# Performance work log

Hardware: AMD Instinct MI355X
Metric: run time of the kernel (lower is better)

Reference implementation:

```python
import jax, jax.numpy as jnp
import numpy as np

N = 100000      # nodes
E = 800000      # directed edges (avg in-degree 8)
FIN = 2         # node features: [type, requests]
C = 32          # embedding_size (per-head out channels)
H = 4           # heads
HC = H * C      # 128
L = 3           # extra conv layers after conv1
D1, D2 = 128, 64
NL = 15         # num_locations
BN_EPS = 1e-5


def _tconv(x, src, dst, ea, qw, qb, kw, kb, vw, vb, ew, skw, skb, bw):
    """PyG TransformerConv with heads=H, concat=True, beta=True, edge_dim."""
    n = x.shape[0]
    q = (x @ qw.T + qb).reshape(n, H, C)
    k = (x @ kw.T + kb).reshape(n, H, C)
    v = (x @ vw.T + vb).reshape(n, H, C)
    e = (ea @ ew.T).reshape(-1, H, C)                     # [E,H,C], lin_edge has no bias
    ke = k[src] + e
    alpha = (q[dst] * ke).sum(-1) / jnp.sqrt(jnp.float32(C))   # [E,H]
    # scatter-softmax over incoming edges of each destination node
    amax = jax.ops.segment_max(alpha, dst, num_segments=n)     # [N,H]
    ex = jnp.exp(alpha - amax[dst])
    denom = jax.ops.segment_sum(ex, dst, num_segments=n)
    attn = ex / jnp.where(denom > 0, denom, 1.0)[dst]
    msg = (v[src] + e) * attn[..., None]                       # [E,H,C]
    out = jax.ops.segment_sum(msg, dst, num_segments=n).reshape(n, HC)
    skip = x @ skw.T + skb                                     # root transform
    beta = jax.nn.sigmoid(jnp.concatenate([out, skip, out - skip], -1) @ bw.T)  # [N,1]
    return beta * skip + (1.0 - beta) * out


def _bn(x, g, b):
    # BatchNorm1d with batch statistics (biased variance), as in torch training math
    mu = x.mean(0)
    var = ((x - mu) ** 2).mean(0)
    return (x - mu) / jnp.sqrt(var + BN_EPS) * g + b


def _forward(node_type, requests, latency, active_mask, edge_index, P):
    (q1_w, q1_b, k1_w, k1_b, v1_w, v1_b, e1_w, skip1_w, skip1_b, beta1_w,
     transf1_w, transf1_b, bn1_g, bn1_b,
     qL_w, qL_b, kL_w, kL_b, vL_w, vL_b, eL_w, skipL_w, skipL_b, betaL_w,
     transfL_w, transfL_b, bnL_g, bnL_b,
     lin1_w, lin1_b, lin2_w, lin2_b, rem_w, rem_b, addp_w, addp_b) = P
    src, dst = edge_index[0], edge_index[1]
    ea = latency[:, None]                                  # [E,1]
    x = jnp.stack([node_type, requests], 1)                # [N,2]
    x = _tconv(x, src, dst, ea, q1_w, q1_b, k1_w, k1_b, v1_w, v1_b,
               e1_w, skip1_w, skip1_b, beta1_w)
    x = _bn(jax.nn.relu(x @ transf1_w.T + transf1_b), bn1_g, bn1_b)
    for i in range(L):
        x = _tconv(x, src, dst, ea, qL_w[i], qL_b[i], kL_w[i], kL_b[i], vL_w[i], vL_b[i],
                   eL_w[i], skipL_w[i], skipL_b[i], betaL_w[i])
        x = _bn(jax.nn.relu(x @ transfL_w[i].T + transfL_b[i]), bnL_g[i], bnL_b[i])
    x = jax.nn.relu(x @ lin1_w.T + lin1_b)                 # dropout(p=0.8) is eval no-op
    x = jax.nn.relu(x @ lin2_w.T + lin2_b)                 # [N,D2]
    mask = active_mask
    head = mask[:NL]
    rm_head = jnp.where(head == 0.0, -jnp.inf, jnp.where(jnp.isneginf(head), 0.0, head))
    remove_mask = mask.at[:NL].set(rm_head)
    removed_logits = (x @ rem_w.T + rem_b)[:, 0] + remove_mask   # [N]
    k1, k2 = jax.random.split(jax.random.key(42))
    action1 = jax.random.categorical(k1, removed_logits)
    mask2 = mask.at[action1].set(0.0)
    proj = jnp.tanh(x[action1] @ addp_w.T + addp_b)              # [D2]
    new_logits = x @ proj + mask2                                # [N]
    action2 = jax.random.categorical(k2, new_logits)
    return removed_logits, new_logits, action1, action2


def setup_inputs() -> dict:
    key = jax.random.key(0)
    ks = iter(jax.random.split(key, 80))
    def nrm(shape, s=0.1):
        return jax.random.normal(next(ks), shape, jnp.float32) * s
    inp = {
        "node_type": jax.random.uniform(next(ks), (N,), jnp.float32),
        "requests": jax.random.uniform(next(ks), (N,), jnp.float32),
        "latency": jax.random.uniform(next(ks), (E,), jnp.float32),
        "active_mask": jnp.zeros((N,), jnp.float32),
        "edge_index": jax.random.randint(next(ks), (2, E), 0, N, dtype=jnp.int32),
        "q1_w": nrm((HC, FIN)), "q1_b": jnp.zeros((HC,)),
        "k1_w": nrm((HC, FIN)), "k1_b": jnp.zeros((HC,)),
        "v1_w": nrm((HC, FIN)), "v1_b": jnp.zeros((HC,)),
        "e1_w": nrm((HC, 1)),
        "skip1_w": nrm((HC, FIN)), "skip1_b": jnp.zeros((HC,)),
        "beta1_w": nrm((1, 3 * HC)),
        "transf1_w": nrm((C, HC)), "transf1_b": jnp.zeros((C,)),
        "bn1_g": jnp.ones((C,)), "bn1_b": jnp.zeros((C,)),
        "qL_w": nrm((L, HC, C)), "qL_b": jnp.zeros((L, HC)),
        "kL_w": nrm((L, HC, C)), "kL_b": jnp.zeros((L, HC)),
        "vL_w": nrm((L, HC, C)), "vL_b": jnp.zeros((L, HC)),
        "eL_w": nrm((L, HC, 1)),
        "skipL_w": nrm((L, HC, C)), "skipL_b": jnp.zeros((L, HC)),
        "betaL_w": nrm((L, 1, 3 * HC)),
        "transfL_w": nrm((L, C, HC)), "transfL_b": jnp.zeros((L, C)),
        "bnL_g": jnp.ones((L, C)), "bnL_b": jnp.zeros((L, C)),
        "lin1_w": nrm((D1, C)), "lin1_b": jnp.zeros((D1,)),
        "lin2_w": nrm((D2, D1)), "lin2_b": jnp.zeros((D2,)),
        "rem_w": nrm((1, D2)), "rem_b": jnp.zeros((1,)),
        "addp_w": nrm((D2, D2)), "addp_b": jnp.zeros((D2,)),
    }
    return inp


def reference(node_type, requests, latency, active_mask, edge_index,
              q1_w, q1_b, k1_w, k1_b, v1_w, v1_b, e1_w, skip1_w, skip1_b, beta1_w,
              transf1_w, transf1_b, bn1_g, bn1_b,
              qL_w, qL_b, kL_w, kL_b, vL_w, vL_b, eL_w, skipL_w, skipL_b, betaL_w,
              transfL_w, transfL_b, bnL_g, bnL_b,
              lin1_w, lin1_b, lin2_w, lin2_b, rem_w, rem_b, addp_w, addp_b):
    P = (q1_w, q1_b, k1_w, k1_b, v1_w, v1_b, e1_w, skip1_w, skip1_b, beta1_w,
         transf1_w, transf1_b, bn1_g, bn1_b,
         qL_w, qL_b, kL_w, kL_b, vL_w, vL_b, eL_w, skipL_w, skipL_b, betaL_w,
         transfL_w, transfL_b, bnL_g, bnL_b,
         lin1_w, lin1_b, lin2_w, lin2_b, rem_w, rem_b, addp_w, addp_b)
    rl, nl, a1, a2 = _forward(node_type, requests, latency, active_mask, edge_index, P)
    log_probs = jnp.stack([jax.nn.log_softmax(rl)[a1], jax.nn.log_softmax(nl)[a2]])
    logits = jnp.stack([rl, nl])      # [2,N]
    actions = jnp.stack([a1, a2])     # [2]
    return logits, actions, log_probs
```

## Files before the change

### kernel.cpp

```cpp
#include <hip/hip_runtime.h>
#include <hip/hip_bf16.h>
#include <math.h>
#include <stdint.h>
#include <limits.h>

#define NN 100000
#define NE 800000
#define PB 512
#define NDB 512
#define NEGBIG (-1e30f)

typedef __hip_bfloat16 bf16;

__device__ __forceinline__ float bf2f(unsigned short u)
{
  union { unsigned v; float f; } x; x.v = ((unsigned)u) << 16; return x.f;
}
__device__ __forceinline__ unsigned short f2bf(float f)
{
  bf16 h = __float2bfloat16(f);
  return *reinterpret_cast<unsigned short*>(&h);
}

__device__ __forceinline__ uint2 tf_dev(unsigned k0, unsigned k1, unsigned x0, unsigned x1)
{
  const unsigned ks2 = k0 ^ k1 ^ 0x1BD11BDAu;
#define TFR(r) { x0 += x1; x1 = (x1 << r) | (x1 >> (32 - r)); x1 ^= x0; }
  x0 += k0; x1 += k1;
  TFR(13) TFR(15) TFR(26) TFR(6)
  x0 += k1; x1 += ks2 + 1u;
  TFR(17) TFR(29) TFR(16) TFR(24)
  x0 += ks2; x1 += k0 + 2u;
  TFR(13) TFR(15) TFR(26) TFR(6)
  x0 += k0; x1 += k1 + 3u;
  TFR(17) TFR(29) TFR(16) TFR(24)
  x0 += k1; x1 += ks2 + 4u;
  TFR(13) TFR(15) TFR(26) TFR(6)
  x0 += ks2; x1 += k0 + 5u;
#undef TFR
  return make_uint2(x0, x1);
}

static void tf_host(unsigned k0, unsigned k1, unsigned x0, unsigned x1,
                    unsigned* o0, unsigned* o1)
{
  const unsigned ks2 = k0 ^ k1 ^ 0x1BD11BDAu;
#define TFR(r) { x0 += x1; x1 = (x1 << r) | (x1 >> (32 - r)); x1 ^= x0; }
  x0 += k0; x1 += k1;
  TFR(13) TFR(15) TFR(26) TFR(6)
  x0 += k1; x1 += ks2 + 1u;
  TFR(17) TFR(29) TFR(16) TFR(24)
  x0 += ks2; x1 += k0 + 2u;
  TFR(13) TFR(15) TFR(26) TFR(6)
  x0 += k0; x1 += k1 + 3u;
  TFR(17) TFR(29) TFR(16) TFR(24)
  x0 += k1; x1 += ks2 + 4u;
  TFR(13) TFR(15) TFR(26) TFR(6)
  x0 += ks2; x1 += k0 + 5u;
#undef TFR
  *o0 = x0; *o1 = x1;
}

__device__ __forceinline__ float gumbel_of(unsigned ka, unsigned kb, int i)
{
  uint2 c = tf_dev(ka, kb, 0u, (unsigned)i);
  unsigned bits = c.x ^ c.y;
  float f = __uint_as_float((bits >> 9) | 0x3f800000u) - 1.0f;
  const float TINYF = 1.17549435e-38f;
  float u = fmaxf(TINYF, f + TINYF);
  return -logf(-logf(u));
}

__global__ __launch_bounds__(256) void k_zero2(int* __restrict__ a, int* __restrict__ b)
{
  int i = blockIdx.x * 256 + threadIdx.x;
  if (i < NN) { a[i] = 0; b[i] = 0; }
}

__global__ __launch_bounds__(256) void k_hist(const int* __restrict__ edst, int* __restrict__ deg)
{
  int e = blockIdx.x * 256 + threadIdx.x;
  if (e < NE) atomicAdd(&deg[edst[e]], 1);
}

__global__ __launch_bounds__(1024) void k_scan(const int* __restrict__ deg, int* __restrict__ rowptr)
{
  __shared__ int wsum[16];
  __shared__ int chtot;
  const int t = threadIdx.x;
  const int lane = t & 63;
  const int wv = t >> 6;
  int carry = 0;
  for (int base = 0; base < NN; base += 4096) {
    int i0 = base + t * 4;
    int d0 = 0, d1 = 0, d2 = 0, d3 = 0;
    if (i0 + 3 < NN) { int4 dd = *(const int4*)(deg + i0); d0 = dd.x; d1 = dd.y; d2 = dd.z; d3 = dd.w; }
    else {
      if (i0     < NN) d0 = deg[i0];
      if (i0 + 1 < NN) d1 = deg[i0 + 1];
      if (i0 + 2 < NN) d2 = deg[i0 + 2];
      if (i0 + 3 < NN) d3 = deg[i0 + 3];
    }
    int tsum = d0 + d1 + d2 + d3;
    int sc = tsum;
    #pragma unroll
    for (int off = 1; off < 64; off <<= 1) { int o = __shfl_up(sc, off); if (lane >= off) sc += o; }
    if (lane == 63) wsum[wv] = sc;
    __syncthreads();
    if (wv == 0 && lane < 16) {
      int wval = wsum[lane];
      int wsc = wval;
      #pragma unroll
      for (int off = 1; off < 16; off <<= 1) { int o = __shfl_up(wsc, off); if (lane >= off) wsc += o; }
      if (lane == 15) chtot = wsc;
      wsum[lane] = wsc - wval;
    }
    __syncthreads();
    int excl = carry + wsum[wv] + (sc - tsum);
    if (i0     < NN) rowptr[i0]     = excl;
    if (i0 + 1 < NN) rowptr[i0 + 1] = excl + d0;
    if (i0 + 2 < NN) rowptr[i0 + 2] = excl + d0 + d1;
    if (i0 + 3 < NN) rowptr[i0 + 3] = excl + d0 + d1 + d2;
    carry += chtot;
    __syncthreads();
  }
  if (t == 0) rowptr[NN] = carry;
}

__global__ __launch_bounds__(256) void k_scatter(
    const int* __restrict__ esrc, const int* __restrict__ edst,
    const float* __restrict__ lat, const int* __restrict__ rowptr,
    int* __restrict__ fill, int2* __restrict__ csr)
{
  int e = blockIdx.x * 256 + threadIdx.x;
  if (e >= NE) return;
  int d = edst[e];
  int pos = rowptr[d] + atomicAdd(&fill[d], 1);
  csr[pos] = make_int2(esrc[e], __float_as_int(lat[e]));
}

__global__ __launch_bounds__(256) void k_qkvs_first(
    const float* __restrict__ nt, const float* __restrict__ rq,
    const float* __restrict__ qw, const float* __restrict__ qbv,
    const float* __restrict__ kw, const float* __restrict__ kbv,
    const float* __restrict__ vw, const float* __restrict__ vbv,
    const float* __restrict__ sw, const float* __restrict__ sbv,
    float* __restrict__ q, unsigned short* __restrict__ kv, float* __restrict__ sk)
{
  int idx = blockIdx.x * 256 + threadIdx.x;
  if (idx >= NN * 64) return;
  int n = idx >> 6, l = idx & 63;
  int j0 = 2 * l, j1 = 2 * l + 1;
  float a = nt[n], b = rq[n];
  float2 qo;
  qo.x = (a * qw[2 * j0] + b * qw[2 * j0 + 1]) + qbv[j0];
  qo.y = (a * qw[2 * j1] + b * qw[2 * j1 + 1]) + qbv[j1];
  ((float2*)q)[idx] = qo;
  ushort4 kvo;
  kvo.x = f2bf((a * kw[2 * j0] + b * kw[2 * j0 + 1]) + kbv[j0]);
  kvo.y = f2bf((a * kw[2 * j1] + b * kw[2 * j1 + 1]) + kbv[j1]);
  kvo.z = f2bf((a * vw[2 * j0] + b * vw[2 * j0 + 1]) + vbv[j0]);
  kvo.w = f2bf((a * vw[2 * j1] + b * vw[2 * j1 + 1]) + vbv[j1]);
  ((ushort4*)kv)[idx] = kvo;
  float2 so;
  so.x = (a * sw[2 * j0] + b * sw[2 * j0 + 1]) + sbv[j0];
  so.y = (a * sw[2 * j1] + b * sw[2 * j1 + 1]) + sbv[j1];
  ((float2*)sk)[idx] = so;
}

__global__ __launch_bounds__(256) void k_qkvs_gen(
    const float* __restrict__ yb, const float* __restrict__ stats,
    const float* __restrict__ bng, const float* __restrict__ bnb,
    const float* __restrict__ wq, const float* __restrict__ bq,
    const float* __restrict__ wk, const float* __restrict__ bk,
    const float* __restrict__ wv, const float* __restrict__ bv,
    const float* __restrict__ wsk, const float* __restrict__ bsk,
    float* __restrict__ oq, unsigned short* __restrict__ okv, float* __restrict__ os)
{
  const int t = threadIdx.x;
  __shared__ __align__(16) float xs[64 * 32];
  const int ch0 = (t * 4) & 31;
  float sc[4], sh[4];
  #pragma unroll
  for (int c = 0; c < 4; ++c) {
    int ch = ch0 + c;
    float rsig = 1.0f / stats[32 + ch];
    sc[c] = bng[ch] * rsig;
    sh[c] = bnb[ch] - stats[ch] * sc[c];
  }
  const int ntiles = (NN + 63) / 64;

  if (blockIdx.y == 1) {
    const int l = t & 63;
    const int slot = t >> 6;
    float wk0[32], wk1[32], wv0[32], wv1[32];
    #pragma unroll
    for (int i = 0; i < 32; ++i) {
      wk0[i] = wk[(2 * l) * 32 + i];
      wk1[i] = wk[(2 * l + 1) * 32 + i];
      wv0[i] = wv[(2 * l) * 32 + i];
      wv1[i] = wv[(2 * l + 1) * 32 + i];
    }
    const float bk0 = bk[2 * l], bk1 = bk[2 * l + 1];
    const float bv0 = bv[2 * l], bv1 = bv[2 * l + 1];
    for (int tile = blockIdx.x; tile < ntiles; tile += gridDim.x) {
      const int base = tile * 64;
      const int remn = (NN - base < 64) ? (NN - base) : 64;
      __syncthreads();
      #pragma unroll
      for (int rep = 0; rep < 2; ++rep) {
        int f = t + rep * 256;
        if (f * 4 < remn * 32) {
          float4 xv = ((const float4*)(yb + (size_t)base * 32))[f];
          xv.x = fmaf(xv.x, sc[0], sh[0]);
          xv.y = fmaf(xv.y, sc[1], sh[1]);
          xv.z = fmaf(xv.z, sc[2], sh[2]);
          xv.w = fmaf(xv.w, sc[3], sh[3]);
          ((float4*)xs)[f] = xv;
        }
      }
      __syncthreads();
      for (int n = 0; n < 16; ++n) {
        int node = base + slot * 16 + n;
        float a0 = 0.f, a1 = 0.f, c0 = 0.f, c1 = 0.f;
        #pragma unroll
        for (int i = 0; i < 32; ++i) {
          float x = xs[(slot * 16 + n) * 32 + i];
          a0 = fmaf(x, wk0[i], a0);
          a1 = fmaf(x, wk1[i], a1);
          c0 = fmaf(x, wv0[i], c0);
          c1 = fmaf(x, wv1[i], c1);
        }
        if (node < NN) {
          ushort4 kvo;
          kvo.x = f2bf(a0 + bk0);
          kvo.y = f2bf(a1 + bk1);
          kvo.z = f2bf(c0 + bv0);
          kvo.w = f2bf(c1 + bv1);
          ((ushort4*)okv)[(size_t)node * 64 + l] = kvo;
        }
      }
    }
  } else {
    const float* W; const float* B; float* Of;
    if (blockIdx.y == 0) { W = wq; B = bq; Of = oq; }
    else { W = wsk; B = bsk; Of = os; }
    const int j = t & 127;
    const int slot = t >> 7;
    float wreg[32];
    #pragma unroll
    for (int i = 0; i < 32; ++i) wreg[i] = W[j * 32 + i];
    const float bj = B[j];
    for (int tile = blockIdx.x; tile < ntiles; tile += gridDim.x) {
      const int base = tile * 64;
      const int remn = (NN - base < 64) ? (NN - base) : 64;
      __syncthreads();
      #pragma unroll
      for (int rep = 0; rep < 2; ++rep) {
        int f = t + rep * 256;
        if (f * 4 < remn * 32) {
          float4 xv = ((const float4*)(yb + (size_t)base * 32))[f];
          xv.x = fmaf(xv.x, sc[0], sh[0]);
          xv.y = fmaf(xv.y, sc[1], sh[1]);
          xv.z = fmaf(xv.z, sc[2], sh[2]);
          xv.w = fmaf(xv.w, sc[3], sh[3]);
          ((float4*)xs)[f] = xv;
        }
      }
      __syncthreads();
      for (int n = 0; n < 32; ++n) {
        int node = base + slot * 32 + n;
        float acc = 0.f;
        #pragma unroll
        for (int i = 0; i < 32; ++i) acc = fmaf(xs[(slot * 32 + n) * 32 + i], wreg[i], acc);
        if (node < NN) Of[(size_t)node * 128 + j] = acc + bj;
      }
    }
  }
}

__global__ __launch_bounds__(256) void k_lin_narrow(
    const float* __restrict__ yb, const float* __restrict__ stats,
    const float* __restrict__ bng, const float* __restrict__ bnb,
    const float* __restrict__ W, const float* __restrict__ B, float* __restrict__ O)
{
  const int t = threadIdx.x;
  const int j = t & 127;
  const int slot = t >> 7;
  float wreg[32];
  #pragma unroll
  for (int i = 0; i < 32; ++i) wreg[i] = W[j * 32 + i];
  const float bj = B[j];
  const int ch0 = (t * 4) & 31;
  float sc[4], sh[4];
  #pragma unroll
  for (int c = 0; c < 4; ++c) {
    int ch = ch0 + c;
    float rsig = 1.0f / stats[32 + ch];
    sc[c] = bng[ch] * rsig;
    sh[c] = bnb[ch] - stats[ch] * sc[c];
  }
  __shared__ __align__(16) float xs[64 * 32];
  const int ntiles = (NN + 63) / 64;
  for (int tile = blockIdx.x; tile < ntiles; tile += gridDim.x) {
    const int base = tile * 64;
    const int remn = (NN - base < 64) ? (NN - base) : 64;
    __syncthreads();
    #pragma unroll
    for (int rep = 0; rep < 2; ++rep) {
      int f = t + rep * 256;
      if (f * 4 < remn * 32) {
        float4 xv = ((const float4*)(yb + (size_t)base * 32))[f];
        xv.x = fmaf(xv.x, sc[0], sh[0]);
        xv.y = fmaf(xv.y, sc[1], sh[1]);
        xv.z = fmaf(xv.z, sc[2], sh[2]);
        xv.w = fmaf(xv.w, sc[3], sh[3]);
        ((float4*)xs)[f] = xv;
      }
    }
    __syncthreads();
    for (int n = 0; n < 32; ++n) {
      int node = base + slot * 32 + n;
      float acc = 0.f;
      #pragma unroll
      for (int i = 0; i < 32; ++i) acc = fmaf(xs[(slot * 32 + n) * 32 + i], wreg[i], acc);
      if (node < NN) O[(size_t)node * 128 + j] = fmaxf(acc + bj, 0.f);
    }
  }
}

#define XPITCH 132
#define WPITCH 130
template<int COUT, bool STATS, bool REM>
__global__ __launch_bounds__(256) void k_dense(
    const float* __restrict__ xin, const float* __restrict__ W,
    const float* __restrict__ bias, float* __restrict__ out,
    double* __restrict__ psum, double* __restrict__ psq,
    const float* __restrict__ rw, const float* __restrict__ rb,
    const float* __restrict__ amask, float* __restrict__ rl)
{
  constexpr int JB = COUT / 16;
  __shared__ __align__(16) float xs[64 * XPITCH];
  __shared__ float Ws[COUT * WPITCH];
  __shared__ float rem_lds[REM ? 16 * 64 : 1];

  const int t = threadIdx.x;
  const int nq = t & 15;
  const int chq = t >> 4;

  for (int idx = t; idx < COUT * 128; idx += 256) {
    int c = idx >> 7, k = idx & 127;
    Ws[c * WPITCH + k] = W[idx];
  }
  float bj[JB];
  float rwj[REM ? JB : 1];
  #pragma unroll
  for (int j = 0; j < JB; ++j) {
    bj[j] = bias[chq * JB + j];
    if (REM) rwj[j] = rw[chq * JB + j];
  }
  double sd[STATS ? JB : 1], sq[STATS ? JB : 1];
  if (STATS) {
    #pragma unroll
    for (int j = 0; j < JB; ++j) { sd[j] = 0.0; sq[j] = 0.0; }
  }

  const int ntiles = (NN + 63) / 64;
  for (int tile = blockIdx.x; tile < ntiles; tile += gridDim.x) {
    const int base = tile * 64;
    __syncthreads();
    #pragma unroll
    for (int r = 0; r < 8; ++r) {
      int f = t + r * 256;
      int n = f >> 5, kq = f & 31;
      int gn = base + n;
      if (gn >= NN) gn = NN - 1;
      float4 v = *(const float4*)(xin + (size_t)gn * 128 + kq * 4);
      *(float4*)(xs + n * XPITCH + kq * 4) = v;
    }
    __syncthreads();

    float acc[4][JB];
    #pragma unroll
    for (int s = 0; s < 4; ++s)
      #pragma unroll
      for (int j = 0; j < JB; ++j) acc[s][j] = bj[j];

    #pragma unroll 8
    for (int k2 = 0; k2 < 64; ++k2) {
      const int k = 2 * k2;
      float2 xv[4];
      #pragma unroll
      for (int s = 0; s < 4; ++s)
        xv[s] = *(const float2*)(xs + (nq + 16 * s) * XPITCH + k);
      float2 wv[JB];
      #pragma unroll
      for (int j = 0; j < JB; ++j)
        wv[j] = *(const float2*)(Ws + (chq * JB + j) * WPITCH + k);
      #pragma unroll
      for (int s = 0; s < 4; ++s)
        #pragma unroll
        for (int j = 0; j < JB; ++j) {
          acc[s][j] = fmaf(xv[s].x, wv[j].x, acc[s][j]);
          acc[s][j] = fmaf(xv[s].y, wv[j].y, acc[s][j]);
        }
    }

    #pragma unroll
    for (int s = 0; s < 4; ++s) {
      const int node = base + nq + 16 * s;
      const bool ok = node < NN;
      #pragma unroll
      for (int j = 0; j < JB; ++j) acc[s][j] = fmaxf(acc[s][j], 0.f);
      if (ok) {
        if (COUT == 32) {
          *(float2*)(out + (size_t)node * 32 + chq * 2) = make_float2(acc[s][0], acc[s][1]);
        } else {
          *(float4*)(out + (size_t)node * 64 + chq * 4) =
              make_float4(acc[s][0], acc[s][1], acc[s][2], acc[s][3]);
        }
      }
      if (STATS && ok) {
        #pragma unroll
        for (int j = 0; j < JB; ++j) {
          sd[j] += (double)acc[s][j];
          sq[j] += (double)acc[s][j] * (double)acc[s][j];
        }
      }
      if (REM) {
        float p = 0.f;
        #pragma unroll
        for (int j = 0; j < JB; ++j) p = fmaf(acc[s][j], rwj[j], p);
        rem_lds[chq * 64 + nq + 16 * s] = p;
      }
    }

    if (REM) {
      __syncthreads();
      if (t < 64) {
        int node = base + t;
        if (node < NN) {
          float v = rb[0];
          #pragma unroll
          for (int c = 0; c < 16; ++c) v += rem_lds[c * 64 + t];
          float mv = amask[node];
          float mterm;
          if (node < 15) mterm = (mv == 0.f) ? -INFINITY : ((mv == -INFINITY) ? 0.f : mv);
          else mterm = mv;
          rl[node] = fmaxf(v + mterm, NEGBIG);
        }
      }
    }
  }

  if (STATS) {
    __shared__ double sred[256 * 2];
    __syncthreads();
    #pragma unroll
    for (int j = 0; j < JB; ++j) { sred[t * 2 + j] = sd[j]; }
    __syncthreads();
    if (t < 32) {
      int cq = t >> 1, j = t & 1;
      double a = 0.0;
      #pragma unroll
      for (int n = 0; n < 16; ++n) a += sred[(cq * 16 + n) * 2 + j];
      psum[blockIdx.x * 32 + t] = a;
    }
    __syncthreads();
    #pragma unroll
    for (int j = 0; j < JB; ++j) { sred[t * 2 + j] = sq[j]; }
    __syncthreads();
    if (t < 32) {
      int cq = t >> 1, j = t & 1;
      double a = 0.0;
      #pragma unroll
      for (int n = 0; n < 16; ++n) a += sred[(cq * 16 + n) * 2 + j];
      psq[blockIdx.x * 32 + t] = a;
    }
  }
}

__global__ __launch_bounds__(1024) void k_stats2(
    const double* __restrict__ psum, const double* __restrict__ psq, float* __restrict__ stats)
{
  const int t = threadIdx.x;
  const int ch = t & 31;
  const int chunk = t >> 5;
  double s = 0.0, q = 0.0;
  for (int b = chunk; b < NDB; b += 32) { s += psum[b * 32 + ch]; q += psq[b * 32 + ch]; }
  __shared__ double rs[1024];
  __shared__ double rq[1024];
  rs[t] = s; rq[t] = q;
  __syncthreads();
  for (int off = 16; off > 0; off >>= 1) {
    if (chunk < off) { rs[t] += rs[t + off * 32]; rq[t] += rq[t + off * 32]; }
    __syncthreads();
  }
  if (t < 32) {
    double mu = rs[t] / (double)NN;
    double var = rq[t] / (double)NN - mu * mu;
    if (var < 0.0) var = 0.0;
    stats[t] = (float)mu;
    stats[32 + t] = sqrtf((float)var + 1e-5f);
  }
}

__global__ __launch_bounds__(256) void k_attn(
    const float* __restrict__ qb, const unsigned short* __restrict__ kvb,
    float* __restrict__ skh,
    const int* __restrict__ rowptr, const int2* __restrict__ csr,
    const float* __restrict__ ew, const float* __restrict__ bw)
{
  const int wid = (blockIdx.x * 256 + threadIdx.x) >> 6;
  const int lane = threadIdx.x & 63;
  if (wid >= NN) return;
  const float2 qv = ((const float2*)qb)[(size_t)wid * 64 + lane];
  const float2 ew2 = ((const float2*)ew)[lane];
  const ushort4* kvp = (const ushort4*)kvb;
  const int p0 = rowptr[wid], p1 = rowptr[wid + 1];

  float m = -INFINITY, s = 0.f, accx = 0.f, accy = 0.f;
  const float iscale = 0.17677669529663689f;

#define EDGE_BODY(cc, kv) {                                            \
    float lat = __int_as_float(cc.y);                                  \
    float e0 = lat * ew2.x, e1 = lat * ew2.y;                          \
    float kx = bf2f(kv.x) + e0, ky = bf2f(kv.y) + e1;                  \
    float part = qv.x * kx + qv.y * ky;                                \
    part += __shfl_xor(part, 1);                                       \
    part += __shfl_xor(part, 2);                                       \
    part += __shfl_xor(part, 4);                                       \
    part += __shfl_xor(part, 8);                                       \
    float alpha = part * iscale;                                       \
    float vx = bf2f(kv.z) + e0, vy = bf2f(kv.w) + e1;                  \
    float mn = fmaxf(m, alpha);                                        \
    float scl = __expf(m - mn);                                        \
    float pt = __expf(alpha - mn);                                     \
    s = fmaf(s, scl, pt);                                              \
    accx = fmaf(accx, scl, pt * vx);                                   \
    accy = fmaf(accy, scl, pt * vy);                                   \
    m = mn; }

  int p = p0;
  for (; p + 3 < p1; p += 4) {
    int2 c0 = csr[p], c1 = csr[p + 1], c2 = csr[p + 2], c3 = csr[p + 3];
    ushort4 kv0 = kvp[(size_t)c0.x * 64 + lane];
    ushort4 kv1 = kvp[(size_t)c1.x * 64 + lane];
    ushort4 kv2 = kvp[(size_t)c2.x * 64 + lane];
    ushort4 kv3 = kvp[(size_t)c3.x * 64 + lane];
    EDGE_BODY(c0, kv0)
    EDGE_BODY(c1, kv1)
    EDGE_BODY(c2, kv2)
    EDGE_BODY(c3, kv3)
  }
  for (; p < p1; ++p) {
    int2 c0 = csr[p];
    ushort4 kv0 = kvp[(size_t)c0.x * 64 + lane];
    EDGE_BODY(c0, kv0)
  }
#undef EDGE_BODY

  float sdiv = (s > 0.f) ? s : 1.f;
  float ox = accx / sdiv, oy = accy / sdiv;

  float2* sk2p = (float2*)skh;
  float2 skv = sk2p[(size_t)wid * 64 + lane];
  const float2* bw2 = (const float2*)bw;
  float2 b1 = bw2[lane], b2 = bw2[64 + lane], b3 = bw2[128 + lane];
  float part = b1.x * ox + b1.y * oy + b2.x * skv.x + b2.y * skv.y
             + b3.x * (ox - skv.x) + b3.y * (oy - skv.y);
  #pragma unroll
  for (int off = 1; off < 64; off <<= 1) part += __shfl_xor(part, off);
  float beta = 1.f / (1.f + __expf(-part));
  float2 hv;
  hv.x = beta * skv.x + (1.f - beta) * ox;
  hv.y = beta * skv.y + (1.f - beta) * oy;
  sk2p[(size_t)wid * 64 + lane] = hv;
}

__global__ __launch_bounds__(256) void k_pass(
    const float* __restrict__ lg,
    float* __restrict__ pm, float* __restrict__ ps, float* __restrict__ pg, int* __restrict__ pidx,
    unsigned ka, unsigned kb)
{
  float m = -INFINITY, s = 0.f, g = -INFINITY; int gi = INT_MAX; bool hg = false;
  for (int i = blockIdx.x * 256 + threadIdx.x; i < NN; i += gridDim.x * 256) {
    float v = lg[i];
    if (v > m) { s = (m == -INFINITY) ? 1.f : fmaf(s, expf(m - v), 1.f); m = v; }
    else if (v != -INFINITY) s += expf(v - m);
    float tot = v + gumbel_of(ka, kb, i);
    if (!hg || tot > g || (tot == g && i < gi)) { g = tot; gi = i; hg = true; }
  }
  __shared__ float sm[256], ss[256], sg[256]; __shared__ int si[256];
  int t = threadIdx.x;
  sm[t] = m; ss[t] = s; sg[t] = g; si[t] = gi;
  __syncthreads();
  for (int off = 128; off > 0; off >>= 1) {
    if (t < off) {
      float m2 = sm[t + off], s2 = ss[t + off];
      float M = fmaxf(sm[t], m2);
      float sn = 0.f;
      if (M != -INFINITY) {
        if (sm[t] != -INFINITY) sn += ss[t] * expf(sm[t] - M);
        if (m2 != -INFINITY) sn += s2 * expf(m2 - M);
      }
      sm[t] = M; ss[t] = sn;
      float g2 = sg[t + off]; int i2 = si[t + off];
      if (g2 > sg[t] || (g2 == sg[t] && i2 < si[t])) { sg[t] = g2; si[t] = i2; }
    }
    __syncthreads();
  }
  if (t == 0) { pm[blockIdx.x] = sm[0]; ps[blockIdx.x] = ss[0]; pg[blockIdx.x] = sg[0]; pidx[blockIdx.x] = si[0]; }
}

__global__ __launch_bounds__(PB) void k_choose(
    const float* __restrict__ lg,
    const float* __restrict__ pm, const float* __restrict__ ps,
    const float* __restrict__ pg, const int* __restrict__ pidx,
    float* __restrict__ act_out, float* __restrict__ lp_out, int* __restrict__ a_scr)
{
  __shared__ float sm[PB], ss[PB], sg[PB]; __shared__ int si[PB];
  int t = threadIdx.x;
  sm[t] = pm[t]; ss[t] = ps[t]; sg[t] = pg[t]; si[t] = pidx[t];
  __syncthreads();
  for (int off = PB / 2; off > 0; off >>= 1) {
    if (t < off) {
      float m2 = sm[t + off], s2 = ss[t + off];
      float M = fmaxf(sm[t], m2);
      float sn = 0.f;
      if (M != -INFINITY) {
        if (sm[t] != -INFINITY) sn += ss[t] * expf(sm[t] - M);
        if (m2 != -INFINITY) sn += s2 * expf(m2 - M);
      }
      sm[t] = M; ss[t] = sn;
      float g2 = sg[t + off]; int i2 = si[t + off];
      if (g2 > sg[t] || (g2 == sg[t] && i2 < si[t])) { sg[t] = g2; si[t] = i2; }
    }
    __syncthreads();
  }
  if (t == 0) {
    int a = si[0];
    a_scr[0] = a;
    act_out[0] = (float)a;
    lp_out[0] = (lg[a] - sm[0]) - logf(ss[0]);
  }
}

__global__ void k_proj(const float* __restrict__ xf, const int* __restrict__ a1p,
                       const float* __restrict__ aw, const float* __restrict__ ab,
                       float* __restrict__ proj)
{
  __shared__ float xs[64];
  int t = threadIdx.x;
  int a1 = a1p[0];
  xs[t] = xf[(size_t)a1 * 64 + t];
  __syncthreads();
  float acc = 0.f;
  #pragma unroll
  for (int i = 0; i < 64; ++i) acc = fmaf(xs[i], aw[t * 64 + i], acc);
  proj[t] = tanhf(acc + ab[t]);
}

__global__ __launch_bounds__(256) void k_nl(
    const float* __restrict__ xf, const float* __restrict__ proj,
    const float* __restrict__ amask, const int* __restrict__ a1p, float* __restrict__ nl)
{
  int wid = (blockIdx.x * 256 + threadIdx.x) >> 6;
  int lane = threadIdx.x & 63;
  if (wid >= NN) return;
  float part = xf[(size_t)wid * 64 + lane] * proj[lane];
  #pragma unroll
  for (int off = 1; off < 64; off <<= 1) part += __shfl_xor(part, off);
  if (lane == 0) {
    int a1 = a1p[0];
    float mv = (wid == a1) ? 0.f : amask[wid];
    nl[wid] = fmaxf(part + mv, NEGBIG);
  }
}

extern "C" void kernel_launch(void* const* d_in, const int* in_sizes, int n_in,
                              void* d_out, int out_size, void* d_ws, size_t ws_size,
                              hipStream_t stream)
{
  (void)in_sizes; (void)n_in; (void)out_size; (void)ws_size;

  const float* node_type = (const float*)d_in[0];
  const float* requests  = (const float*)d_in[1];
  const float* latency   = (const float*)d_in[2];
  const float* amask     = (const float*)d_in[3];
  const int*   eidx      = (const int*)d_in[4];
  const int* esrc = eidx;
  const int* edst = eidx + NE;

  const float* q1_w = (const float*)d_in[5];  const float* q1_b = (const float*)d_in[6];
  const float* k1_w = (const float*)d_in[7];  const float* k1_b = (const float*)d_in[8];
  const float* v1_w = (const float*)d_in[9];  const float* v1_b = (const float*)d_in[10];
  const float* e1_w = (const float*)d_in[11];
  const float* sk1_w = (const float*)d_in[12]; const float* sk1_b = (const float*)d_in[13];
  const float* be1_w = (const float*)d_in[14];
  const float* tf1_w = (const float*)d_in[15]; const float* tf1_b = (const float*)d_in[16];
  const float* bn1_g = (const float*)d_in[17]; const float* bn1_b = (const float*)d_in[18];
  const float* qL_w = (const float*)d_in[19]; const float* qL_b = (const float*)d_in[20];
  const float* kL_w = (const float*)d_in[21]; const float* kL_b = (const float*)d_in[22];
  const float* vL_w = (const float*)d_in[23]; const float* vL_b = (const float*)d_in[24];
  const float* eL_w = (const float*)d_in[25];
  const float* skL_w = (const float*)d_in[26]; const float* skL_b = (const float*)d_in[27];
  const float* beL_w = (const float*)d_in[28];
  const float* tfL_w = (const float*)d_in[29]; const float* tfL_b = (const float*)d_in[30];
  const float* bnL_g = (const float*)d_in[31]; const float* bnL_b = (const float*)d_in[32];
  const float* l1_w = (const float*)d_in[33]; const float* l1_b = (const float*)d_in[34];
  const float* l2_w = (const float*)d_in[35]; const float* l2_b = (const float*)d_in[36];
  const float* rem_w = (const float*)d_in[37]; const float* rem_b = (const float*)d_in[38];
  const float* ap_w = (const float*)d_in[39]; const float* ap_b = (const float*)d_in[40];

  char* ws = (char*)d_ws;
  size_t off = 0;
  auto alloc = [&](size_t bytes) -> void* {
    void* p = ws + off;
    off += (bytes + 255) & ~(size_t)255;
    return p;
  };
  float* qbuf = (float*)alloc((size_t)NN * 128 * 4);
  unsigned short* kvbuf = (unsigned short*)alloc((size_t)NN * 256 * 2);
  float* skb  = (float*)alloc((size_t)NN * 128 * 4);
  float* yb   = (float*)alloc((size_t)NN * 32 * 4);
  int*   rowptr = (int*)alloc((size_t)(NN + 1) * 4);
  int*   deg    = (int*)alloc((size_t)NN * 4);
  int*   fill   = (int*)alloc((size_t)NN * 4);
  int2*  csr    = (int2*)alloc((size_t)NE * 8);
  double* psum = (double*)alloc((size_t)NDB * 32 * 8);
  double* psq  = (double*)alloc((size_t)NDB * 32 * 8);
  float* stats = (float*)alloc(64 * 4);
  float* pm = (float*)alloc(PB * 4);
  float* ps = (float*)alloc(PB * 4);
  float* pg = (float*)alloc(PB * 4);
  int*   pidx = (int*)alloc(PB * 4);
  float* proj = (float*)alloc(64 * 4);
  int*   a_scr = (int*)alloc(2 * 4);
  float* y1 = qbuf;
  float* xf = (float*)kvbuf;

  unsigned k1a, k1b, k2a, k2b;
  tf_host(0u, 42u, 0u, 0u, &k1a, &k1b);
  tf_host(0u, 42u, 0u, 1u, &k2a, &k2b);

  float* dout = (float*)d_out;

  k_zero2<<<(NN + 255) / 256, 256, 0, stream>>>(deg, fill);
  k_hist<<<(NE + 255) / 256, 256, 0, stream>>>(edst, deg);
  k_scan<<<1, 1024, 0, stream>>>(deg, rowptr);
  k_scatter<<<(NE + 255) / 256, 256, 0, stream>>>(esrc, edst, latency, rowptr, fill, csr);

  k_qkvs_first<<<(NN * 64 + 255) / 256, 256, 0, stream>>>(
      node_type, requests, q1_w, q1_b, k1_w, k1_b, v1_w, v1_b, sk1_w, sk1_b,
      qbuf, kvbuf, skb);
  k_attn<<<NN / 4, 256, 0, stream>>>(qbuf, kvbuf, skb, rowptr, csr, e1_w, be1_w);
  k_dense<32, true, false><<<NDB, 256, 0, stream>>>(skb, tf1_w, tf1_b, yb, psum, psq,
                                                    nullptr, nullptr, nullptr, nullptr);
  k_stats2<<<1, 1024, 0, stream>>>(psum, psq, stats);

  for (int i = 0; i < 3; ++i) {
    const float* g = (i == 0) ? bn1_g : bnL_g + (i - 1) * 32;
    const float* b = (i == 0) ? bn1_b : bnL_b + (i - 1) * 32;
    k_qkvs_gen<<<dim3(256, 3), 256, 0, stream>>>(
        yb, stats, g, b,
        qL_w + i * 4096, qL_b + i * 128,
        kL_w + i * 4096, kL_b + i * 128,
        vL_w + i * 4096, vL_b + i * 128,
        skL_w + i * 4096, skL_b + i * 128,
        qbuf, kvbuf, skb);
    k_attn<<<NN / 4, 256, 0, stream>>>(qbuf, kvbuf, skb, rowptr, csr,
                                       eL_w + i * 128, beL_w + i * 384);
    k_dense<32, true, false><<<NDB, 256, 0, stream>>>(skb, tfL_w + i * 4096, tfL_b + i * 32,
                                                      yb, psum, psq,
                                                      nullptr, nullptr, nullptr, nullptr);
    k_stats2<<<1, 1024, 0, stream>>>(psum, psq, stats);
  }

  k_lin_narrow<<<512, 256, 0, stream>>>(yb, stats, bnL_g + 2 * 32, bnL_b + 2 * 32, l1_w, l1_b, y1);
  k_dense<64, false, true><<<NDB, 256, 0, stream>>>(y1, l2_w, l2_b, xf, nullptr, nullptr,
                                                    rem_w, rem_b, amask, dout);

  k_pass<<<PB, 256, 0, stream>>>(dout, pm, ps, pg, pidx, k1a, k1b);
  k_choose<<<1, PB, 0, stream>>>(dout, pm, ps, pg, pidx,
                                 dout + 2 * NN, dout + 2 * NN + 2, a_scr);
  k_proj<<<1, 64, 0, stream>>>(xf, a_scr, ap_w, ap_b, proj);
  k_nl<<<NN / 4, 256, 0, stream>>>(xf, proj, amask, a_scr, dout + NN);
  k_pass<<<PB, 256, 0, stream>>>(dout + NN, pm, ps, pg, pidx, k2a, k2b);
  k_choose<<<1, PB, 0, stream>>>(dout + NN, pm, ps, pg, pidx,
                                 dout + 2 * NN + 1, dout + 2 * NN + 3, a_scr + 1);
}
```

Measured before the change: 947.3 us.

## Register-tile node projections with LDS weights and drop softmax max tracking

```diff
diff --git a/kernel.cpp b/kernel.cpp
--- a/kernel.cpp
+++ b/kernel.cpp
@@ -20,6 +20,10 @@
 {
   bf16 h = __float2bfloat16(f);
   return *reinterpret_cast<unsigned short*>(&h);
+}
+__device__ __forceinline__ unsigned pk2(float a, float b)
+{
+  return (unsigned)f2bf(a) | ((unsigned)f2bf(b) << 16);
 }
 
 __device__ __forceinline__ uint2 tf_dev(unsigned k0, unsigned k1, unsigned x0, unsigned x1)
@@ -168,7 +172,9 @@
   ((float2*)sk)[idx] = so;
 }
 
-__global__ __launch_bounds__(256) void k_qkvs_gen(
+#define QP 36
+#define WP 33
+__global__ __launch_bounds__(256) void k_qkvs3(
     const float* __restrict__ yb, const float* __restrict__ stats,
     const float* __restrict__ bng, const float* __restrict__ bnb,
     const float* __restrict__ wq, const float* __restrict__ bq,
@@ -177,9 +183,29 @@
     const float* __restrict__ wsk, const float* __restrict__ bsk,
     float* __restrict__ oq, unsigned short* __restrict__ okv, float* __restrict__ os)
 {
+  __shared__ __align__(16) float xs[64 * QP];
+  __shared__ __align__(16) float Wl[2 * 128 * WP];
+
   const int t = threadIdx.x;
-  __shared__ __align__(16) float xs[64 * 32];
-  const int ch0 = (t * 4) & 31;
+  const int nq = t & 15;
+  const int chq = t >> 4;
+  const int y = blockIdx.y;
+
+  if (y == 1) {
+    for (int idx = t; idx < 128 * 32; idx += 256) {
+      int c = idx >> 5, k = idx & 31;
+      Wl[c * WP + k] = wk[idx];
+      Wl[128 * WP + c * WP + k] = wv[idx];
+    }
+  } else {
+    const float* W = (y == 0) ? wq : wsk;
+    for (int idx = t; idx < 128 * 32; idx += 256) {
+      int c = idx >> 5, k = idx & 31;
+      Wl[c * WP + k] = W[idx];
+    }
+  }
+
+  const int ch0 = (t & 7) * 4;
   float sc[4], sh[4];
   #pragma unroll
   for (int c = 0; c < 4; ++c) {
@@ -188,110 +214,117 @@
     sc[c] = bng[ch] * rsig;
     sh[c] = bnb[ch] - stats[ch] * sc[c];
   }
+
   const int ntiles = (NN + 63) / 64;
-
-  if (blockIdx.y == 1) {
-    const int l = t & 63;
-    const int slot = t >> 6;
-    float wk0[32], wk1[32], wv0[32], wv1[32];
-    #pragma unroll
-    for (int i = 0; i < 32; ++i) {
-      wk0[i] = wk[(2 * l) * 32 + i];
-      wk1[i] = wk[(2 * l + 1) * 32 + i];
-      wv0[i] = wv[(2 * l) * 32 + i];
-      wv1[i] = wv[(2 * l + 1) * 32 + i];
-    }
-    const float bk0 = bk[2 * l], bk1 = bk[2 * l + 1];
-    const float bv0 = bv[2 * l], bv1 = bv[2 * l + 1];
-    for (int tile = blockIdx.x; tile < ntiles; tile += gridDim.x) {
-      const int base = tile * 64;
-      const int remn = (NN - base < 64) ? (NN - base) : 64;
-      __syncthreads();
-      #pragma unroll
-      for (int rep = 0; rep < 2; ++rep) {
-        int f = t + rep * 256;
-        if (f * 4 < remn * 32) {
-          float4 xv = ((const float4*)(yb + (size_t)base * 32))[f];
-          xv.x = fmaf(xv.x, sc[0], sh[0]);
-          xv.y = fmaf(xv.y, sc[1], sh[1]);
-          xv.z = fmaf(xv.z, sc[2], sh[2]);
-          xv.w = fmaf(xv.w, sc[3], sh[3]);
-          ((float4*)xs)[f] = xv;
+  for (int tile = blockIdx.x; tile < ntiles; tile += gridDim.x) {
+    const int base = tile * 64;
+    __syncthreads();
+    #pragma unroll
+    for (int rep = 0; rep < 2; ++rep) {
+      int f = t + rep * 256;
+      int n = f >> 3, kq = f & 7;
+      int gn = base + n;
+      if (gn >= NN) gn = NN - 1;
+      float4 v = *(const float4*)(yb + (size_t)gn * 32 + kq * 4);
+      v.x = fmaf(v.x, sc[0], sh[0]);
+      v.y = fmaf(v.y, sc[1], sh[1]);
+      v.z = fmaf(v.z, sc[2], sh[2]);
+      v.w = fmaf(v.w, sc[3], sh[3]);
+      *(float4*)(xs + n * QP + kq * 4) = v;
+    }
+    __syncthreads();
+
+    if (y == 1) {
+      float ak[4][8], av[4][8];
+      #pragma unroll
+      for (int s = 0; s < 4; ++s)
+        #pragma unroll
+        for (int j = 0; j < 8; ++j) { ak[s][j] = bk[chq * 8 + j]; av[s][j] = bv[chq * 8 + j]; }
+      #pragma unroll 4
+      for (int k2 = 0; k2 < 16; ++k2) {
+        const int k = 2 * k2;
+        float2 xv[4];
+        #pragma unroll
+        for (int s = 0; s < 4; ++s) xv[s] = *(const float2*)(xs + (nq + 16 * s) * QP + k);
+        #pragma unroll
+        for (int j = 0; j < 8; ++j) {
+          float2 wk2 = *(const float2*)(Wl + (chq * 8 + j) * WP + k);
+          float2 wv2 = *(const float2*)(Wl + 128 * WP + (chq * 8 + j) * WP + k);
+          #pragma unroll
+          for (int s = 0; s < 4; ++s) {
+            ak[s][j] = fmaf(xv[s].x, wk2.x, ak[s][j]);
+            ak[s][j] = fmaf(xv[s].y, wk2.y, ak[s][j]);
+            av[s][j] = fmaf(xv[s].x, wv2.x, av[s][j]);
+            av[s][j] = fmaf(xv[s].y, wv2.y, av[s][j]);
+          }
         }
       }
-      __syncthreads();
-      for (int n = 0; n < 16; ++n) {
-        int node = base + slot * 16 + n;
-        float a0 = 0.f, a1 = 0.f, c0 = 0.f, c1 = 0.f;
-        #pragma unroll
-        for (int i = 0; i < 32; ++i) {
-          float x = xs[(slot * 16 + n) * 32 + i];
-          a0 = fmaf(x, wk0[i], a0);
-          a1 = fmaf(x, wk1[i], a1);
-          c0 = fmaf(x, wv0[i], c0);
-          c1 = fmaf(x, wv1[i], c1);
+      #pragma unroll
+      for (int s = 0; s < 4; ++s) {
+        int node = base + nq + 16 * s;
+        if (node < NN) {
+          uint4 A, B;
+          A.x = pk2(ak[s][0], ak[s][1]); A.y = pk2(av[s][0], av[s][1]);
+          A.z = pk2(ak[s][2], ak[s][3]); A.w = pk2(av[s][2], av[s][3]);
+          B.x = pk2(ak[s][4], ak[s][5]); B.y = pk2(av[s][4], av[s][5]);
+          B.z = pk2(ak[s][6], ak[s][7]); B.w = pk2(av[s][6], av[s][7]);
+          unsigned short* dst = okv + (size_t)node * 256 + chq * 16;
+          *(uint4*)dst = A;
+          *(uint4*)(dst + 8) = B;
         }
+      }
+    } else {
+      float* Of = (y == 0) ? oq : os;
+      const float* B = (y == 0) ? bq : bsk;
+      float acc[4][8];
+      #pragma unroll
+      for (int s = 0; s < 4; ++s)
+        #pragma unroll
+        for (int j = 0; j < 8; ++j) acc[s][j] = B[chq * 8 + j];
+      #pragma unroll 4
+      for (int k2 = 0; k2 < 16; ++k2) {
+        const int k = 2 * k2;
+        float2 xv[4];
+        #pragma unroll
+        for (int s = 0; s < 4; ++s) xv[s] = *(const float2*)(xs + (nq + 16 * s) * QP + k);
+        #pragma unroll
+        for (int j = 0; j < 8; ++j) {
+          float2 w2 = *(const float2*)(Wl + (chq * 8 + j) * WP + k);
+          #pragma unroll
+          for (int s = 0; s < 4; ++s) {
+            acc[s][j] = fmaf(xv[s].x, w2.x, acc[s][j]);
+            acc[s][j] = fmaf(xv[s].y, w2.y, acc[s][j]);
+          }
+        }
+      }
+      #pragma unroll
+      for (int s = 0; s < 4; ++s) {
+        int node = base + nq + 16 * s;
         if (node < NN) {
-          ushort4 kvo;
-          kvo.x = f2bf(a0 + bk0);
-          kvo.y = f2bf(a1 + bk1);
-          kvo.z = f2bf(c0 + bv0);
-          kvo.w = f2bf(c1 + bv1);
-          ((ushort4*)okv)[(size_t)node * 64 + l] = kvo;
+          float* dst = Of + (size_t)node * 128 + chq * 8;
+          *(float4*)dst = make_float4(acc[s][0], acc[s][1], acc[s][2], acc[s][3]);
+          *(float4*)(dst + 4) = make_float4(acc[s][4], acc[s][5], acc[s][6], acc[s][7]);
         }
       }
     }
-  } else {
-    const float* W; const float* B; float* Of;
-    if (blockIdx.y == 0) { W = wq; B = bq; Of = oq; }
-    else { W = wsk; B = bsk; Of = os; }
-    const int j = t & 127;
-    const int slot = t >> 7;
-    float wreg[32];
-    #pragma unroll
-    for (int i = 0; i < 32; ++i) wreg[i] = W[j * 32 + i];
-    const float bj = B[j];
-    for (int tile = blockIdx.x; tile < ntiles; tile += gridDim.x) {
-      const int base = tile * 64;
-      const int remn = (NN - base < 64) ? (NN - base) : 64;
-      __syncthreads();
-      #pragma unroll
-      for (int rep = 0; rep < 2; ++rep) {
-        int f = t + rep * 256;
-        if (f * 4 < remn * 32) {
-          float4 xv = ((const float4*)(yb + (size_t)base * 32))[f];
-          xv.x = fmaf(xv.x, sc[0], sh[0]);
-          xv.y = fmaf(xv.y, sc[1], sh[1]);
-          xv.z = fmaf(xv.z, sc[2], sh[2]);
-          xv.w = fmaf(xv.w, sc[3], sh[3]);
-          ((float4*)xs)[f] = xv;
-        }
-      }
-      __syncthreads();
-      for (int n = 0; n < 32; ++n) {
-        int node = base + slot * 32 + n;
-        float acc = 0.f;
-        #pragma unroll
-        for (int i = 0; i < 32; ++i) acc = fmaf(xs[(slot * 32 + n) * 32 + i], wreg[i], acc);
-        if (node < NN) Of[(size_t)node * 128 + j] = acc + bj;
-      }
-    }
-  }
-}
-
-__global__ __launch_bounds__(256) void k_lin_narrow(
+  }
+}
+
+__global__ __launch_bounds__(256) void k_lin1d(
     const float* __restrict__ yb, const float* __restrict__ stats,
     const float* __restrict__ bng, const float* __restrict__ bnb,
     const float* __restrict__ W, const float* __restrict__ B, float* __restrict__ O)
 {
+  __shared__ __align__(16) float xs[64 * QP];
+  __shared__ __align__(16) float Wl[128 * WP];
   const int t = threadIdx.x;
-  const int j = t & 127;
-  const int slot = t >> 7;
-  float wreg[32];
-  #pragma unroll
-  for (int i = 0; i < 32; ++i) wreg[i] = W[j * 32 + i];
-  const float bj = B[j];
-  const int ch0 = (t * 4) & 31;
+  const int nq = t & 15;
+  const int chq = t >> 4;
+  for (int idx = t; idx < 128 * 32; idx += 256) {
+    int c = idx >> 5, k = idx & 31;
+    Wl[c * WP + k] = W[idx];
+  }
+  const int ch0 = (t & 7) * 4;
   float sc[4], sh[4];
   #pragma unroll
   for (int c = 0; c < 4; ++c) {
@@ -300,31 +333,55 @@
     sc[c] = bng[ch] * rsig;
     sh[c] = bnb[ch] - stats[ch] * sc[c];
   }
-  __shared__ __align__(16) float xs[64 * 32];
   const int ntiles = (NN + 63) / 64;
   for (int tile = blockIdx.x; tile < ntiles; tile += gridDim.x) {
     const int base = tile * 64;
-    const int remn = (NN - base < 64) ? (NN - base) : 64;
     __syncthreads();
     #pragma unroll
     for (int rep = 0; rep < 2; ++rep) {
       int f = t + rep * 256;
-      if (f * 4 < remn * 32) {
-        float4 xv = ((const float4*)(yb + (size_t)base * 32))[f];
-        xv.x = fmaf(xv.x, sc[0], sh[0]);
-        xv.y = fmaf(xv.y, sc[1], sh[1]);
-        xv.z = fmaf(xv.z, sc[2], sh[2]);
-        xv.w = fmaf(xv.w, sc[3], sh[3]);
-        ((float4*)xs)[f] = xv;
-      }
-    }
-    __syncthreads();
-    for (int n = 0; n < 32; ++n) {
-      int node = base + slot * 32 + n;
-      float acc = 0.f;
-      #pragma unroll
-      for (int i = 0; i < 32; ++i) acc = fmaf(xs[(slot * 32 + n) * 32 + i], wreg[i], acc);
-      if (node < NN) O[(size_t)node * 128 + j] = fmaxf(acc + bj, 0.f);
+      int n = f >> 3, kq = f & 7;
+      int gn = base + n;
+      if (gn >= NN) gn = NN - 1;
+      float4 v = *(const float4*)(yb + (size_t)gn * 32 + kq * 4);
+      v.x = fmaf(v.x, sc[0], sh[0]);
+      v.y = fmaf(v.y, sc[1], sh[1]);
+      v.z = fmaf(v.z, sc[2], sh[2]);
+      v.w = fmaf(v.w, sc[3], sh[3]);
+      *(float4*)(xs + n * QP + kq * 4) = v;
+    }
+    __syncthreads();
+    float acc[4][8];
+    #pragma unroll
+    for (int s = 0; s < 4; ++s)
+      #pragma unroll
+      for (int j = 0; j < 8; ++j) acc[s][j] = B[chq * 8 + j];
+    #pragma unroll 4
+    for (int k2 = 0; k2 < 16; ++k2) {
+      const int k = 2 * k2;
+      float2 xv[4];
+      #pragma unroll
+      for (int s = 0; s < 4; ++s) xv[s] = *(const float2*)(xs + (nq + 16 * s) * QP + k);
+      #pragma unroll
+      for (int j = 0; j < 8; ++j) {
+        float2 w2 = *(const float2*)(Wl + (chq * 8 + j) * WP + k);
+        #pragma unroll
+        for (int s = 0; s < 4; ++s) {
+          acc[s][j] = fmaf(xv[s].x, w2.x, acc[s][j]);
+          acc[s][j] = fmaf(xv[s].y, w2.y, acc[s][j]);
+        }
+      }
+    }
+    #pragma unroll
+    for (int s = 0; s < 4; ++s) {
+      int node = base + nq + 16 * s;
+      if (node < NN) {
+        float* dst = O + (size_t)node * 128 + chq * 8;
+        *(float4*)dst = make_float4(fmaxf(acc[s][0], 0.f), fmaxf(acc[s][1], 0.f),
+                                    fmaxf(acc[s][2], 0.f), fmaxf(acc[s][3], 0.f));
+        *(float4*)(dst + 4) = make_float4(fmaxf(acc[s][4], 0.f), fmaxf(acc[s][5], 0.f),
+                                          fmaxf(acc[s][6], 0.f), fmaxf(acc[s][7], 0.f));
+      }
     }
   }
 }
@@ -519,7 +576,7 @@
   const ushort4* kvp = (const ushort4*)kvb;
   const int p0 = rowptr[wid], p1 = rowptr[wid + 1];
 
-  float m = -INFINITY, s = 0.f, accx = 0.f, accy = 0.f;
+  float s = 0.f, accx = 0.f, accy = 0.f;
   const float iscale = 0.17677669529663689f;
 
 #define EDGE_BODY(cc, kv) {                                            \
@@ -531,15 +588,11 @@
     part += __shfl_xor(part, 2);                                       \
     part += __shfl_xor(part, 4);                                       \
     part += __shfl_xor(part, 8);                                       \
-    float alpha = part * iscale;                                       \
+    float pt = __expf(part * iscale);                                  \
     float vx = bf2f(kv.z) + e0, vy = bf2f(kv.w) + e1;                  \
-    float mn = fmaxf(m, alpha);                                        \
-    float scl = __expf(m - mn);                                        \
-    float pt = __expf(alpha - mn);                                     \
-    s = fmaf(s, scl, pt);                                              \
-    accx = fmaf(accx, scl, pt * vx);                                   \
-    accy = fmaf(accy, scl, pt * vy);                                   \
-    m = mn; }
+    s += pt;                                                           \
+    accx = fmaf(pt, vx, accx);                                         \
+    accy = fmaf(pt, vy, accy); }
 
   int p = p0;
   for (; p + 3 < p1; p += 4) {
@@ -762,7 +815,7 @@
   for (int i = 0; i < 3; ++i) {
     const float* g = (i == 0) ? bn1_g : bnL_g + (i - 1) * 32;
     const float* b = (i == 0) ? bn1_b : bnL_b + (i - 1) * 32;
-    k_qkvs_gen<<<dim3(256, 3), 256, 0, stream>>>(
+    k_qkvs3<<<dim3(NDB, 3), 256, 0, stream>>>(
         yb, stats, g, b,
         qL_w + i * 4096, qL_b + i * 128,
         kL_w + i * 4096, kL_b + i * 128,
@@ -777,7 +830,7 @@
     k_stats2<<<1, 1024, 0, stream>>>(psum, psq, stats);
   }
 
-  k_lin_narrow<<<512, 256, 0, stream>>>(yb, stats, bnL_g + 2 * 32, bnL_b + 2 * 32, l1_w, l1_b, y1);
+  k_lin1d<<<NDB, 256, 0, stream>>>(yb, stats, bnL_g + 2 * 32, bnL_b + 2 * 32, l1_w, l1_b, y1);
   k_dense<64, false, true><<<NDB, 256, 0, stream>>>(y1, l2_w, l2_b, xf, nullptr, nullptr,
                                                     rem_w, rem_b, amask, dout);
 
```

Measured after the change: 886.9 us. 1.07x faster.
